# Performance work log

Measured on AMD Instinct MI355X. Metric: run time of the kernel, lower is better.

Reference implementation:

```python
import jax, jax.numpy as jnp
import numpy as np

B, T, C, H = 8, 2048, 1024, 64  # batch, seq (== block_size), n_embd, head_size


def setup_inputs() -> dict:
    key = jax.random.key(0)
    k1, k2, k3, k4 = jax.random.split(key, 4)
    x = jax.random.normal(k1, (B, T, C), dtype=jnp.float32)
    scale = 0.02
    Wk = jax.random.normal(k2, (H, C), dtype=jnp.float32) * scale  # nn.Linear weight [out,in]
    Wq = jax.random.normal(k3, (H, C), dtype=jnp.float32) * scale
    Wv = jax.random.normal(k4, (H, C), dtype=jnp.float32) * scale
    return {"x": x, "Wk": Wk, "Wq": Wq, "Wv": Wv}


def reference(x, Wk, Wq, Wv):
    # k, q, v projections (bias-free linears): x @ W.T
    k = jnp.einsum('btc,hc->bth', x, Wk)
    q = jnp.einsum('btc,hc->bth', x, Wq)
    v = jnp.einsum('btc,hc->bth', x, Wv)
    # NOTE: source MULTIPLIES by sqrt(head_size) (faithful to original code)
    wei = jnp.einsum('bth,bsh->bts', q, k) * (H ** 0.5)  # [B,T,T]
    causal = jnp.tril(jnp.ones((T, T), dtype=bool))
    wei = jnp.where(causal, wei, -jnp.inf)
    wei = jax.nn.softmax(wei, axis=-1)
    # dropout_value = 0.0 -> identity (deterministic baseline)
    out = jnp.einsum('bts,bsh->bth', wei, v)  # [B,T,H]
    return out
```

## Files before the change

### kernel.cpp

```cpp
#include <hip/hip_runtime.h>

#define BB 8
#define TT 2048
#define CC 1024
#define HH 64
#define MM (BB * TT)

typedef _Float16 half8 __attribute__((ext_vector_type(8)));
typedef _Float16 half4 __attribute__((ext_vector_type(4)));
typedef float floatx4 __attribute__((ext_vector_type(4)));

template <int CTRL>
__device__ __forceinline__ float dpp_max_step(float x)
{
    union { float f; int i; } u, v;
    u.f = x;
    v.i = __builtin_amdgcn_update_dpp(u.i, u.i, CTRL, 0xf, 0xf, false);
    return fmaxf(x, v.f);
}
__device__ __forceinline__ float rowmax16(float x)
{
    x = dpp_max_step<0x128>(x);
    x = dpp_max_step<0x124>(x);
    x = dpp_max_step<0x122>(x);
    x = dpp_max_step<0x121>(x);
    return x;
}

__device__ __forceinline__ void gll16h(const _Float16* g, _Float16* l)
{
    __builtin_amdgcn_global_load_lds(
        (const __attribute__((address_space(1))) unsigned int*)g,
        (__attribute__((address_space(3))) unsigned int*)l, 16, 0, 0);
}

#define MEMFENCE asm volatile("" ::: "memory")

__global__ __launch_bounds__(256)
void w_pack(const float* __restrict__ Wk, const float* __restrict__ Wq,
            const float* __restrict__ Wv, _Float16* __restrict__ Wp)
{
    const int T   = blockIdx.x * 256 + threadIdx.x;
    const int c   = T / 768;
    const int rem = T - c * 768;
    const int nf  = rem >> 6;
    const int l   = rem & 63;
    const int col = nf * 16 + (l & 15);
    const int k   = c * 32 + (l >> 4) * 8;
    const int which = col >> 6;
    const float* __restrict__ src = (which == 0) ? Wq : ((which == 1) ? Wk : Wv);
    const float scale = (which == 0) ? 8.0f : 1.0f;
    const int srow = col & 63;
    const float4 a = *reinterpret_cast<const float4*>(&src[srow * 1024 + k]);
    const float4 b = *reinterpret_cast<const float4*>(&src[srow * 1024 + k + 4]);
    const half8 o = { (_Float16)(a.x * scale), (_Float16)(a.y * scale),
                      (_Float16)(a.z * scale), (_Float16)(a.w * scale),
                      (_Float16)(b.x * scale), (_Float16)(b.y * scale),
                      (_Float16)(b.z * scale), (_Float16)(b.w * scale) };
    *reinterpret_cast<half8*>(&Wp[(size_t)T * 8]) = o;
}

__global__ __launch_bounds__(512, 1)
void qkv13(const float* __restrict__ x, const _Float16* __restrict__ Wp,
           _Float16* __restrict__ q16, _Float16* __restrict__ Kp,
           _Float16* __restrict__ Vp)
{
    __shared__ _Float16 Ws[2][12288];

    const int tid  = threadIdx.x;
    const int lane = tid & 63;
    const int w    = tid >> 6;
    const int blk  = blockIdx.x;
    const int m_base = blk * 64;
    const int fm = lane & 15;
    const int fq = lane >> 4;
    const int fk = fq * 8;
    const int fr = fq * 4;
    const int wm = w >> 2;
    const int wn = w & 3;

    const float* xr0 = &x[(size_t)(m_base + wm * 32 + fm) * CC + fk];
    const float* xr1 = xr0 + 16 * CC;

    const _Float16* wsrc = Wp + lane * 8;

    floatx4 acc[2][3];
    #pragma unroll
    for (int a = 0; a < 2; ++a)
        #pragma unroll
        for (int n = 0; n < 3; ++n)
            #pragma unroll
            for (int r = 0; r < 4; ++r) acc[a][n][r] = 0.0f;

    float4 xA[8], xB[8];

#define STAGE_W(i, slot) do {                                                  \
        const size_t fb = (size_t)(24 * (i) + 3 * w) * 512;                    \
        gll16h(wsrc + fb,        &Ws[slot][(3 * w + 0) * 512]);                \
        gll16h(wsrc + fb + 512,  &Ws[slot][(3 * w + 1) * 512]);                \
        gll16h(wsrc + fb + 1024, &Ws[slot][(3 * w + 2) * 512]);                \
    } while (0)

#define LOAD_X(i, XB) do {                                                     \
        _Pragma("unroll")                                                      \
        for (int a = 0; a < 2; ++a) {                                          \
            const float* xr = a ? xr1 : xr0;                                   \
            _Pragma("unroll")                                                  \
            for (int sub = 0; sub < 2; ++sub) {                                \
                XB[a * 4 + sub * 2 + 0] = *reinterpret_cast<const float4*>(    \
                    xr + (i) * 64 + sub * 32);                                 \
                XB[a * 4 + sub * 2 + 1] = *reinterpret_cast<const float4*>(    \
                    xr + (i) * 64 + sub * 32 + 4);                             \
            }                                                                  \
        }                                                                      \
    } while (0)

#define COMPUTE(sl, XB) do {                                                   \
        half8 wf[2][3];                                                        \
        _Pragma("unroll")                                                      \
        for (int sub = 0; sub < 2; ++sub)                                      \
            _Pragma("unroll")                                                  \
            for (int n = 0; n < 3; ++n)                                        \
                wf[sub][n] = *reinterpret_cast<const half8*>(                  \
                    &Ws[sl][(sub * 12 + wn * 3 + n) * 512 + lane * 8]);        \
        _Pragma("unroll")                                                      \
        for (int a = 0; a < 2; ++a)                                            \
            _Pragma("unroll")                                                  \
            for (int sub = 0; sub < 2; ++sub) {                                \
                const float4 v0 = XB[a * 4 + sub * 2 + 0];                     \
                const float4 v1 = XB[a * 4 + sub * 2 + 1];                     \
                const half8 af = { (_Float16)v0.x, (_Float16)v0.y,             \
                                   (_Float16)v0.z, (_Float16)v0.w,             \
                                   (_Float16)v1.x, (_Float16)v1.y,             \
                                   (_Float16)v1.z, (_Float16)v1.w };           \
                _Pragma("unroll")                                              \
                for (int n = 0; n < 3; ++n)                                    \
                    acc[a][n] = __builtin_amdgcn_mfma_f32_16x16x32_f16(        \
                        af, wf[sub][n], acc[a][n], 0, 0, 0);                   \
            }                                                                  \
    } while (0)

#define QITER(i, XC, XN) do {                                                  \
        STAGE_W((i) + 1, ((i) + 1) & 1);                                       \
        MEMFENCE;                        \
        LOAD_X((i) + 1, XN);                                                   \
        MEMFENCE;                                                              \
        COMPUTE((i) & 1, XC);                                                  \
        asm volatile("s_waitcnt vmcnt(8)" ::: "memory");                       \
        __builtin_amdgcn_s_barrier();                                          \
        MEMFENCE;                                                              \
    } while (0)

    MEMFENCE;
    STAGE_W(0, 0);
    MEMFENCE;
    LOAD_X(0, xA);
    MEMFENCE;
    asm volatile("s_waitcnt vmcnt(8)" ::: "memory");
    __builtin_amdgcn_s_barrier();
    MEMFENCE;

    for (int ii = 0; ii < 7; ++ii) {
        QITER(2 * ii,     xA, xB);
        QITER(2 * ii + 1, xB, xA);
    }
    QITER(14, xA, xB);
    COMPUTE(1, xB);

#undef STAGE_W
#undef LOAD_X
#undef COMPUTE
#undef QITER

    #pragma unroll
    for (int a = 0; a < 2; ++a) {
        const int mt = blk * 4 + wm * 2 + a;
        #pragma unroll
        for (int n = 0; n < 3; ++n) {
            const int col = wn * 48 + n * 16 + fm;
            if (col < 64) {
                #pragma unroll
                for (int r = 0; r < 4; ++r)
                    q16[(size_t)(mt * 16 + fr + r) * HH + col] = (_Float16)acc[a][n][r];
            } else if (col < 128) {
                const int h = col - 64;
                _Float16* kp = &Kp[(size_t)(mt * 2 + (h >> 5)) * 512 + (h & 31)];
                #pragma unroll
                for (int r = 0; r < 4; ++r)
                    kp[(fr + r) * 32] = (_Float16)acc[a][n][r];
            } else {
                const int h = col - 128;
                const half4 pk = { (_Float16)acc[a][n][0], (_Float16)acc[a][n][1],
                                   (_Float16)acc[a][n][2], (_Float16)acc[a][n][3] };
                *reinterpret_cast<half4*>(
                    &Vp[(size_t)((mt >> 2) * 4 + (h >> 4)) * 1024 +
                        ((mt >> 1) & 1) * 512 + fm * 32 + (mt & 1) * 16 + fr]) = pk;
            }
        }
    }
}

__global__ __launch_bounds__(256, 3)
void attn8(const _Float16* __restrict__ q16, const _Float16* __restrict__ Kp,
           const _Float16* __restrict__ Vp, float* __restrict__ out,
           _Float16* __restrict__ Op, float* __restrict__ ml)
{
    __shared__ _Float16 Kls[2][4][1024];
    __shared__ _Float16 Vls[2][4][1024];
    __shared__ _Float16 Ps[4][16 * 68];

    const int bid = blockIdx.x;
    const int g   = 31 - bid / 24;
    const int sub = bid - (31 - g) * 24;
    const int b   = sub & 7;
    const int s   = sub >> 3;

    const int tid  = threadIdx.x;
    const int lane = tid & 63;
    const int w    = tid >> 6;
    const int it   = g * 4 + w;
    const int fm = lane & 15;
    const int fq = lane >> 4;
    const int fk = fq * 8;
    const int fr = fq * 4;

    const int Ji = g + 1;
    const int qq = Ji / 3, rem = Ji - qq * 3;
    const int cnt   = qq + (s < rem ? 1 : 0);
    const int start = s * qq + (s < rem ? s : rem);

    const _Float16* __restrict__ kpb = Kp + (size_t)b * TT * HH;
    const _Float16* __restrict__ vpb = Vp + (size_t)b * TT * HH;

    const int qrow = (b * 128 + it) * 16 + fm;
    const half8 qf0 = *reinterpret_cast<const half8*>(&q16[(size_t)qrow * HH + fk]);
    const half8 qf1 = *reinterpret_cast<const half8*>(&q16[(size_t)qrow * HH + 32 + fk]);

    floatx4 O[4], lacc;
    float m_r[4];
    #pragma unroll
    for (int r = 0; r < 4; ++r) {
        m_r[r] = -3.0e38f;
        lacc[r] = 0.0f;
        #pragma unroll
        for (int ht = 0; ht < 4; ++ht) O[ht][r] = 0.0f;
    }
    const half8 ones = { (_Float16)1.f, (_Float16)1.f, (_Float16)1.f, (_Float16)1.f,
                         (_Float16)1.f, (_Float16)1.f, (_Float16)1.f, (_Float16)1.f };

    const int sperm = ((lane & 15) * 4 + (lane >> 4)) * 8;

    if (cnt > 0) {
        {
            const _Float16* kgp = &kpb[(size_t)(start * 4 + w) * 1024];
            const _Float16* vgp = &vpb[(size_t)(start * 4 + w) * 1024];
            gll16h(kgp + sperm,       &Kls[0][w][0]);
            gll16h(kgp + 512 + sperm, &Kls[0][w][512]);
            gll16h(vgp + sperm,       &Vls[0][w][0]);
            gll16h(vgp + 512 + sperm, &Vls[0][w][512]);
        }
        asm volatile("s_waitcnt vmcnt(0)" ::: "memory");
        __builtin_amdgcn_s_barrier();
        MEMFENCE;

        int buf = 0;
        for (int js = 0; js < cnt; ++js) {
            const int jj = start + js;

            if (js + 1 < cnt) {
                const _Float16* kgp = &kpb[(size_t)((jj + 1) * 4 + w) * 1024];
                const _Float16* vgp = &vpb[(size_t)((jj + 1) * 4 + w) * 1024];
                gll16h(kgp + sperm,       &Kls[buf ^ 1][w][0]);
                gll16h(kgp + 512 + sperm, &Kls[buf ^ 1][w][512]);
                gll16h(vgp + sperm,       &Vls[buf ^ 1][w][0]);
                gll16h(vgp + 512 + sperm, &Vls[buf ^ 1][w][512]);
            }
            MEMFENCE;

            floatx4 sa[4];
            #pragma unroll
            for (int nt = 0; nt < 4; ++nt) {
                #pragma unroll
                for (int r = 0; r < 4; ++r) sa[nt][r] = 0.0f;
                const half8 b0 = *reinterpret_cast<const half8*>(&Kls[buf][nt][lane * 8]);
                const half8 b1 = *reinterpret_cast<const half8*>(&Kls[buf][nt][512 + lane * 8]);
                sa[nt] = __builtin_amdgcn_mfma_f32_16x16x32_f16(qf0, b0, sa[nt], 0, 0, 0);
                sa[nt] = __builtin_amdgcn_mfma_f32_16x16x32_f16(qf1, b1, sa[nt], 0, 0, 0);
            }

            if (jj == g) {
                const int rbase = it * 16 + fr;
                #pragma unroll
                for (int nt = 0; nt < 4; ++nt) {
                    const int col = jj * 64 + nt * 16 + fm;
                    #pragma unroll
                    for (int r = 0; r < 4; ++r)
                        if (col > rbase + r) sa[nt][r] = -3.0e38f;
                }
            }

            #pragma unroll
            for (int r = 0; r < 4; ++r) {
                float mx = fmaxf(fmaxf(sa[0][r], sa[1][r]), fmaxf(sa[2][r], sa[3][r]));
                mx = rowmax16(mx);
                const float mn = fmaxf(m_r[r], mx);
                const float alpha = __expf(m_r[r] - mn);
                m_r[r] = mn;
                _Float16* pp = &Ps[w][(fr + r) * 68 + fm];
                pp[0]  = (_Float16)__expf(sa[0][r] - mn);
                pp[16] = (_Float16)__expf(sa[1][r] - mn);
                pp[32] = (_Float16)__expf(sa[2][r] - mn);
                pp[48] = (_Float16)__expf(sa[3][r] - mn);
                lacc[r] *= alpha;
                O[0][r] *= alpha; O[1][r] *= alpha; O[2][r] *= alpha; O[3][r] *= alpha;
            }

            #pragma unroll
            for (int ch = 0; ch < 2; ++ch) {
                const half8 pa = *reinterpret_cast<const half8*>(&Ps[w][fm * 68 + ch * 32 + fk]);
                lacc = __builtin_amdgcn_mfma_f32_16x16x32_f16(pa, ones, lacc, 0, 0, 0);
                #pragma unroll
                for (int ht = 0; ht < 4; ++ht) {
                    const half8 vb = *reinterpret_cast<const half8*>(
                        &Vls[buf][ht][ch * 512 + lane * 8]);
                    O[ht] = __builtin_amdgcn_mfma_f32_16x16x32_f16(pa, vb, O[ht], 0, 0, 0);
                }
            }

            asm volatile("s_waitcnt vmcnt(0)" ::: "memory");
            __builtin_amdgcn_s_barrier();
            MEMFENCE;
            buf ^= 1;
        }
    }

    #pragma unroll
    for (int r = 0; r < 4; ++r) {
        const int grow = (b * 128 + it) * 16 + fr + r;
        if (s == 0) {
            #pragma unroll
            for (int ht = 0; ht < 4; ++ht)
                out[(size_t)grow * HH + ht * 16 + fm] = O[ht][r];
        } else {
            #pragma unroll
            for (int ht = 0; ht < 4; ++ht)
                Op[((size_t)(s - 1) * MM + grow) * HH + ht * 16 + fm] = (_Float16)O[ht][r];
        }
        if (fm == 0) {
            ml[((size_t)s * MM + grow) * 2 + 0] = m_r[r];
            ml[((size_t)s * MM + grow) * 2 + 1] = lacc[r];
        }
    }
}

__global__ __launch_bounds__(256)
void combine(float* __restrict__ out, const _Float16* __restrict__ Op,
             const float* __restrict__ ml)
{
    const int tid  = threadIdx.x;
    const int grow = blockIdx.x * 64 + (tid >> 2);
    const int c0   = (tid & 3) * 16;

    const float m0 = ml[(size_t)grow * 2 + 0];
    const float l0 = ml[(size_t)grow * 2 + 1];
    const float m1 = ml[((size_t)MM + grow) * 2 + 0];
    const float l1 = ml[((size_t)MM + grow) * 2 + 1];
    const float m2 = ml[((size_t)2 * MM + grow) * 2 + 0];
    const float l2 = ml[((size_t)2 * MM + grow) * 2 + 1];

    const float M  = fmaxf(m0, fmaxf(m1, m2));
    const float w0 = __expf(m0 - M);
    const float w1 = __expf(m1 - M);
    const float w2 = __expf(m2 - M);
    const float inv = 1.0f / (w0 * l0 + w1 * l1 + w2 * l2);

    #pragma unroll
    for (int i = 0; i < 16; i += 4) {
        float4 o0 = *reinterpret_cast<float4*>(&out[(size_t)grow * HH + c0 + i]);
        const half4 h1 = *reinterpret_cast<const half4*>(&Op[(size_t)grow * HH + c0 + i]);
        const half4 h2 = *reinterpret_cast<const half4*>(&Op[(size_t)MM * HH + (size_t)grow * HH + c0 + i]);
        o0.x = (w0 * o0.x + w1 * (float)h1[0] + w2 * (float)h2[0]) * inv;
        o0.y = (w0 * o0.y + w1 * (float)h1[1] + w2 * (float)h2[1]) * inv;
        o0.z = (w0 * o0.z + w1 * (float)h1[2] + w2 * (float)h2[2]) * inv;
        o0.w = (w0 * o0.w + w1 * (float)h1[3] + w2 * (float)h2[3]) * inv;
        *reinterpret_cast<float4*>(&out[(size_t)grow * HH + c0 + i]) = o0;
    }
}

extern "C" void kernel_launch(void* const* d_in, const int* in_sizes, int n_in,
                              void* d_out, int out_size, void* d_ws, size_t ws_size,
                              hipStream_t stream)
{
    (void)in_sizes; (void)n_in; (void)out_size; (void)ws_size;

    const float* x  = (const float*)d_in[0];
    const float* Wk = (const float*)d_in[1];
    const float* Wq = (const float*)d_in[2];
    const float* Wv = (const float*)d_in[3];
    float* out = (float*)d_out;

    _Float16* base = (_Float16*)d_ws;
    _Float16* q16 = base;
    _Float16* Kp  = base + (size_t)MM * HH;
    _Float16* Vp  = base + (size_t)2 * MM * HH;
    _Float16* Wp  = base + (size_t)3 * MM * HH;
    _Float16* Op  = Wp + 192 * 1024;
    float*    ml  = (float*)(Op + (size_t)2 * MM * HH);

    w_pack<<<dim3(96), dim3(256), 0, stream>>>(Wk, Wq, Wv, Wp);
    qkv13<<<dim3(256), dim3(512), 0, stream>>>(x, Wp, q16, Kp, Vp);
    attn8<<<dim3(768), dim3(256), 0, stream>>>(q16, Kp, Vp, out, Op, ml);
    combine<<<dim3(256), dim3(256), 0, stream>>>(out, Op, ml);
}
```

Baseline: 147.1 us.

## Triple-buffer K/V staging in attention with two-tile lookahead prefetch

Grows the K/V shared-memory ring from two to three slots and issues direct-to-LDS loads two tiles ahead, waiting with vmcnt(4) so only the oldest tile must have landed. The goal is to hide more global-load latency behind the QK/PV MFMA work. It also skips the barrier after the final tile. The larger LDS footprint comes with lowering the launch-bounds occupancy hint from 3 to 2 blocks per CU, which reduces latency hiding across blocks.

```diff
diff --git a/kernel.cpp b/kernel.cpp
--- a/kernel.cpp
+++ b/kernel.cpp
@@ -200,13 +200,13 @@
     }
 }
 
-__global__ __launch_bounds__(256, 3)
-void attn8(const _Float16* __restrict__ q16, const _Float16* __restrict__ Kp,
+__global__ __launch_bounds__(256, 2)
+void attn9(const _Float16* __restrict__ q16, const _Float16* __restrict__ Kp,
            const _Float16* __restrict__ Vp, float* __restrict__ out,
            _Float16* __restrict__ Op, float* __restrict__ ml)
 {
-    __shared__ _Float16 Kls[2][4][1024];
-    __shared__ _Float16 Vls[2][4][1024];
+    __shared__ _Float16 Kls[3][4][1024];
+    __shared__ _Float16 Vls[3][4][1024];
     __shared__ _Float16 Ps[4][16 * 68];
 
     const int bid = blockIdx.x;
@@ -250,31 +250,32 @@
 
     const int sperm = ((lane & 15) * 4 + (lane >> 4)) * 8;
 
+#define STAGE(jx, sl) do {                                                     \
+        const _Float16* kgp = &kpb[(size_t)((jx) * 4 + w) * 1024];             \
+        const _Float16* vgp = &vpb[(size_t)((jx) * 4 + w) * 1024];             \
+        gll16h(kgp + sperm,       &Kls[sl][w][0]);                             \
+        gll16h(kgp + 512 + sperm, &Kls[sl][w][512]);                           \
+        gll16h(vgp + sperm,       &Vls[sl][w][0]);                             \
+        gll16h(vgp + 512 + sperm, &Vls[sl][w][512]);                           \
+    } while (0)
+
     if (cnt > 0) {
-        {
-            const _Float16* kgp = &kpb[(size_t)(start * 4 + w) * 1024];
-            const _Float16* vgp = &vpb[(size_t)(start * 4 + w) * 1024];
-            gll16h(kgp + sperm,       &Kls[0][w][0]);
-            gll16h(kgp + 512 + sperm, &Kls[0][w][512]);
-            gll16h(vgp + sperm,       &Vls[0][w][0]);
-            gll16h(vgp + 512 + sperm, &Vls[0][w][512]);
+        MEMFENCE;
+        STAGE(start, 0);
+        if (cnt > 1) {
+            STAGE(start + 1, 1);
+            asm volatile("s_waitcnt vmcnt(4)" ::: "memory");
+        } else {
+            asm volatile("s_waitcnt vmcnt(0)" ::: "memory");
         }
-        asm volatile("s_waitcnt vmcnt(0)" ::: "memory");
         __builtin_amdgcn_s_barrier();
         MEMFENCE;
 
-        int buf = 0;
         for (int js = 0; js < cnt; ++js) {
             const int jj = start + js;
-
-            if (js + 1 < cnt) {
-                const _Float16* kgp = &kpb[(size_t)((jj + 1) * 4 + w) * 1024];
-                const _Float16* vgp = &vpb[(size_t)((jj + 1) * 4 + w) * 1024];
-                gll16h(kgp + sperm,       &Kls[buf ^ 1][w][0]);
-                gll16h(kgp + 512 + sperm, &Kls[buf ^ 1][w][512]);
-                gll16h(vgp + sperm,       &Vls[buf ^ 1][w][0]);
-                gll16h(vgp + 512 + sperm, &Vls[buf ^ 1][w][512]);
-            }
+            const int sl = js % 3;
+
+            if (js + 2 < cnt) STAGE(jj + 2, (js + 2) % 3);
             MEMFENCE;
 
             floatx4 sa[4];
@@ -282,8 +283,8 @@
             for (int nt = 0; nt < 4; ++nt) {
                 #pragma unroll
                 for (int r = 0; r < 4; ++r) sa[nt][r] = 0.0f;
-                const half8 b0 = *reinterpret_cast<const half8*>(&Kls[buf][nt][lane * 8]);
-                const half8 b1 = *reinterpret_cast<const half8*>(&Kls[buf][nt][512 + lane * 8]);
+                const half8 b0 = *reinterpret_cast<const half8*>(&Kls[sl][nt][lane * 8]);
+                const half8 b1 = *reinterpret_cast<const half8*>(&Kls[sl][nt][512 + lane * 8]);
                 sa[nt] = __builtin_amdgcn_mfma_f32_16x16x32_f16(qf0, b0, sa[nt], 0, 0, 0);
                 sa[nt] = __builtin_amdgcn_mfma_f32_16x16x32_f16(qf1, b1, sa[nt], 0, 0, 0);
             }
@@ -322,17 +323,22 @@
                 #pragma unroll
                 for (int ht = 0; ht < 4; ++ht) {
                     const half8 vb = *reinterpret_cast<const half8*>(
-                        &Vls[buf][ht][ch * 512 + lane * 8]);
+                        &Vls[sl][ht][ch * 512 + lane * 8]);
                     O[ht] = __builtin_amdgcn_mfma_f32_16x16x32_f16(pa, vb, O[ht], 0, 0, 0);
                 }
             }
 
-            asm volatile("s_waitcnt vmcnt(0)" ::: "memory");
-            __builtin_amdgcn_s_barrier();
-            MEMFENCE;
-            buf ^= 1;
+            if (js + 1 < cnt) {
+                if (js + 2 < cnt)
+                    asm volatile("s_waitcnt vmcnt(4)" ::: "memory");
+                else
+                    asm volatile("s_waitcnt vmcnt(0)" ::: "memory");
+                __builtin_amdgcn_s_barrier();
+                MEMFENCE;
+            }
         }
     }
+#undef STAGE
 
     #pragma unroll
     for (int r = 0; r < 4; ++r) {
@@ -409,6 +415,6 @@
 
     w_pack<<<dim3(96), dim3(256), 0, stream>>>(Wk, Wq, Wv, Wp);
     qkv13<<<dim3(256), dim3(512), 0, stream>>>(x, Wp, q16, Kp, Vp);
-    attn8<<<dim3(768), dim3(256), 0, stream>>>(q16, Kp, Vp, out, Op, ml);
+    attn9<<<dim3(768), dim3(256), 0, stream>>>(q16, Kp, Vp, out, Op, ml);
     combine<<<dim3(256), dim3(256), 0, stream>>>(out, Op, ml);
 }
```

Result: no change. 148.1 us (+0.7%).
